# Performance work log

Hardware: AMD Instinct MI355X
Metric: run time of the kernel (lower is better)

The kernel has to match this reference:

```python
import jax, jax.numpy as jnp
import numpy as np

EPS = 1e-5  # torch BatchNorm2d default eps


def _bn(x, gamma, beta, mean, var):
    # inference-mode BatchNorm2d: x [B,C,H,W], params [C]
    inv = gamma / jnp.sqrt(var + EPS)
    return x * inv[None, :, None, None] + (beta - mean * inv)[None, :, None, None]


def _conv1x1(x, W, b=None):
    # 1x1 conv == per-pixel matmul. x [B,C,H,W], W [O,C]
    y = jnp.einsum('bchw,oc->bohw', x, W)
    if b is not None:
        y = y + b[None, :, None, None]
    return y


def _resize_bilinear_ac(x, H, W):
    # bilinear upsample with align_corners=True, separable gather + lerp
    h, w = x.shape[2], x.shape[3]
    ys = jnp.linspace(0.0, h - 1.0, H)
    xs = jnp.linspace(0.0, w - 1.0, W)
    y0 = jnp.floor(ys).astype(jnp.int32); y1 = jnp.minimum(y0 + 1, h - 1)
    x0 = jnp.floor(xs).astype(jnp.int32); x1 = jnp.minimum(x0 + 1, w - 1)
    wy = (ys - y0).astype(x.dtype)
    wx = (xs - x0).astype(x.dtype)
    rows = x[:, :, y0, :] * (1 - wy)[None, None, :, None] + x[:, :, y1, :] * wy[None, None, :, None]
    out = rows[:, :, :, x0] * (1 - wx) + rows[:, :, :, x1] * wx
    return out


def setup_inputs() -> dict:
    key = jax.random.key(0)
    ks = jax.random.split(key, 11)
    B, C, H, W = 8, 512, 96, 96
    Kd, Vd, Od = 256, 256, 512
    s = lambda k, shape: jax.random.normal(k, shape, jnp.float32)
    return dict(
        x=s(ks[0], (B, C, H, W)),
        Wk=s(ks[1], (Kd, C)) * 0.05,                      # shared query/key 1x1 conv
        k_gamma=jnp.ones((Kd,), jnp.float32), k_beta=jnp.zeros((Kd,), jnp.float32),
        k_mean=s(ks[2], (Kd,)) * 0.1, k_var=jnp.abs(s(ks[3], (Kd,))) + 0.5,
        Wv=s(ks[4], (Vd, C)) * 0.05, bv=s(ks[5], (Vd,)) * 0.05,   # value 1x1 conv
        Ww=s(ks[6], (Od, Vd)) * 0.05, bw=s(ks[7], (Od,)) * 0.05,  # 'weights' 1x1 conv (random instead of zero-init so output is nontrivial)
        Wr=s(ks[8], (Od, Od)) * 0.05,                             # refine 1x1 conv (in_dim==out_dim)
        r_gamma=jnp.ones((Od,), jnp.float32), r_beta=jnp.zeros((Od,), jnp.float32),
        r_mean=s(ks[9], (Od,)) * 0.1, r_var=jnp.abs(s(ks[10], (Od,))) + 0.5,
    )


def reference(x, Wk, k_gamma, k_beta, k_mean, k_var, Wv, bv, Ww, bw, Wr, r_gamma, r_beta, r_mean, r_var):
    B, C, H, W = x.shape
    scale = 2
    key_dim = Wk.shape[0]
    # MaxPool2d(scale, scale)
    xp = jax.lax.reduce_window(x, -jnp.inf, jax.lax.max,
                               (1, 1, scale, scale), (1, 1, scale, scale), 'VALID')
    h, w = xp.shape[2], xp.shape[3]
    N = h * w
    # query and key share the same conv+BN+ReLU (func_query = func_key)
    qk = jax.nn.relu(_bn(_conv1x1(xp, Wk), k_gamma, k_beta, k_mean, k_var)).reshape(B, key_dim, N)
    value = _conv1x1(xp, Wv, bv).reshape(B, -1, N)  # [B,Vd,N]
    # sim_map[b,n,m] = <query_n, key_m>, scaled then softmax over m
    sim = jnp.einsum('bkn,bkm->bnm', qk, qk) * (key_dim ** -0.5)
    attn = jax.nn.softmax(sim, axis=-1)
    ctx = jnp.einsum('bnm,bvm->bvn', attn, value).reshape(B, -1, h, w)  # [B,Vd,h,w]
    ctx = _conv1x1(ctx, Ww, bw)                      # -> [B,out_dim,h,w]
    ctx = _resize_bilinear_ac(ctx, H, W)             # align_corners=True bilinear
    out = jax.nn.relu(_bn(_conv1x1(ctx, Wr), r_gamma, r_beta, r_mean, r_var))
    return out
```

## Files before the change

kernel.cpp:

```cpp
#include <hip/hip_runtime.h>
#include <math.h>

typedef __attribute__((ext_vector_type(8))) short bf16x8;
typedef __attribute__((ext_vector_type(4))) float f32x4;

namespace {

constexpr int B_ = 8, C_ = 512, H_ = 96, W_ = 96;
constexpr int HP = 48, WP = 48, N_ = HP * WP;
constexpr int KD = 256, VD = 256, OD = 512;
constexpr int NSPLIT = 4;
constexpr float EPSV = 1e-5f;
constexpr float LOG2E = 1.44269504088896f;

constexpr size_t BOFF_XPT = 0;
constexpr size_t BOFF_QKT = BOFF_XPT + (size_t)B_ * N_ * C_ * 2;
constexpr size_t BOFF_VAL = BOFF_QKT + (size_t)B_ * N_ * KD * 2;
constexpr size_t BOFF_CTX = BOFF_VAL + (size_t)B_ * VD * N_ * 2;
constexpr size_t BOFF_W2  = BOFF_CTX + (size_t)B_ * N_ * VD * 2;
constexpr size_t BOFF_WF  = BOFF_W2  + (size_t)512 * 512 * 2;
constexpr size_t BOFF_BF  = BOFF_WF  + (size_t)OD * VD * 2;
constexpr size_t BOFF_PRT = BOFF_BF  + (size_t)OD * 4;
constexpr size_t BOFF_PM  = BOFF_PRT + (size_t)NSPLIT * B_ * N_ * VD * 2;
constexpr size_t BOFF_PL  = BOFF_PM  + (size_t)NSPLIT * B_ * N_ * 4;

}

__device__ __forceinline__ ushort f2bf(float f) {
    union { float f; unsigned u; } x; x.f = f;
    unsigned r = x.u + 0x7FFFu + ((x.u >> 16) & 1u);
    return (ushort)(r >> 16);
}

__device__ __forceinline__ float bf2f(ushort u) {
    union { unsigned u; float f; } x; x.u = ((unsigned)u) << 16;
    return x.f;
}

__device__ __forceinline__ void gload_lds16(const void* g, void* l) {
    __builtin_amdgcn_global_load_lds(
        (const __attribute__((address_space(1))) unsigned int*)g,
        (__attribute__((address_space(3))) unsigned int*)l, 16, 0, 0);
}

__global__ __launch_bounds__(192) void pool_t_kernel(const float* __restrict__ x,
                                                     ushort* __restrict__ xpT) {
    __shared__ float ps[64][49];
    const int gid = blockIdx.x;
    const int ct = gid & 7;
    const int tmp = gid >> 3;
    const int oh = tmp % 48;
    const int b  = tmp / 48;
    const int t = threadIdx.x;
    const int ow = t % 48, ci = t / 48;

    const int c0 = ct * 64;
#pragma unroll
    for (int pass = 0; pass < 16; ++pass) {
        const int c = pass * 4 + ci;
        const float* px = x + (((size_t)b * C_ + c0 + c) * H_ + 2 * oh) * W_ + 2 * ow;
        float2 a = *reinterpret_cast<const float2*>(px);
        float2 d = *reinterpret_cast<const float2*>(px + W_);
        ps[c][ow] = fmaxf(fmaxf(a.x, a.y), fmaxf(d.x, d.y));
    }
    __syncthreads();
    const int cc2 = (t & 31) * 2;
    const int nr0 = t >> 5;
#pragma unroll
    for (int pass = 0; pass < 8; ++pass) {
        const int nr = pass * 6 + nr0;
        ushort2 p2;
        p2.x = f2bf(ps[cc2][nr]);
        p2.y = f2bf(ps[cc2 + 1][nr]);
        *reinterpret_cast<ushort2*>(&xpT[((size_t)b * N_ + oh * 48 + nr) * C_ + c0 + cc2]) = p2;
    }
}

__global__ __launch_bounds__(256) void prep_kernel(const float* __restrict__ Wk,
                                                   const float* __restrict__ Wv,
                                                   const float* __restrict__ Wr,
                                                   const float* __restrict__ Ww,
                                                   const float* __restrict__ bw,
                                                   ushort* __restrict__ W2,
                                                   ushort* __restrict__ Wfb,
                                                   float* __restrict__ bfb) {
    const int blk = blockIdx.x;
    if (blk < 512) {
        const int m = blk;
        const float* src = (m < 256) ? (Wk + (size_t)m * 512) : (Wv + (size_t)(m - 256) * 512);
        const int k = threadIdx.x * 2;
        float2 v = *reinterpret_cast<const float2*>(src + k);
        ushort2 p; p.x = f2bf(v.x); p.y = f2bf(v.y);
        *reinterpret_cast<ushort2*>(&W2[(size_t)m * 512 + k]) = p;
    } else if (blk < 1024) {
        const int o = blk - 512;
        const int v = threadIdx.x;
        float s = 0.f;
        for (int c = 0; c < OD; ++c)
            s = fmaf(Wr[(size_t)o * OD + c], Ww[(size_t)c * VD + v], s);
        Wfb[(size_t)o * VD + v] = f2bf(s);
    } else {
        const int o = (blk - 1024) * 256 + threadIdx.x;
        float s = 0.f;
        for (int c = 0; c < OD; ++c) s = fmaf(Wr[(size_t)o * OD + c], bw[c], s);
        bfb[o] = s;
    }
}

__global__ __launch_bounds__(256) void qkv_mfma(
    const ushort* __restrict__ W2, const ushort* __restrict__ xpT,
    const float* __restrict__ kg, const float* __restrict__ kb,
    const float* __restrict__ km, const float* __restrict__ kv,
    const float* __restrict__ bv,
    ushort* __restrict__ qkT, ushort* __restrict__ val) {
    __shared__ ushort Al[2][4096];
    __shared__ ushort Bl[2][4096];

    const int id = blockIdx.x;
    const int b = id & 7;
    const int t = id >> 3;
    const int my = t & 7;
    const int nx = t >> 3;
    const int w = threadIdx.x >> 6, l = threadIdx.x & 63;
    const int lr = l & 15, lg = l >> 4;
    const int rbq = (lg * 8) ^ (((lr >> 1) & 3) << 3);

    const ushort* srcA = W2 + (size_t)(my * 64) * 512;
    const ushort* srcB = xpT + ((size_t)b * N_ + nx * 64) * 512;

    auto stage64 = [&](const ushort* src, int koff, char* lbase) {
#pragma unroll
        for (int j = 0; j < 2; ++j) {
            const int prow = j * 64 + w * 16 + (l >> 2);
            const int row = prow & 63;
            const int kc = prow >> 6;
            const int cb = ((l & 3) * 16) ^ (((row >> 1) & 3) << 4);
            const char* s = (const char*)(src + (size_t)row * 512 + koff) + kc * 64 + cb;
            gload_lds16(s, lbase + j * 4096 + w * 1024);
        }
    };

    stage64(srcA, 0, (char*)&Al[0][0]);
    stage64(srcB, 0, (char*)&Bl[0][0]);
    stage64(srcA, 64, (char*)&Al[1][0]);
    stage64(srcB, 64, (char*)&Bl[1][0]);

    f32x4 acc[4];
#pragma unroll
    for (int nt = 0; nt < 4; ++nt) acc[nt] = (f32x4){0.f, 0.f, 0.f, 0.f};

    for (int ks = 0; ks < 8; ++ks) {
        if (ks < 7) { asm volatile("s_waitcnt vmcnt(4)" ::: "memory"); }
        else        { asm volatile("s_waitcnt vmcnt(0)" ::: "memory"); }
        __builtin_amdgcn_s_barrier();
        __builtin_amdgcn_sched_barrier(0);
        const ushort* Ab = &Al[ks & 1][0];
        const ushort* Bb = &Bl[ks & 1][0];
        __builtin_amdgcn_s_setprio(1);
#pragma unroll
        for (int kc = 0; kc < 2; ++kc) {
            bf16x8 af = *reinterpret_cast<const bf16x8*>(Ab + kc * 2048 + (w * 16 + lr) * 32 + rbq);
#pragma unroll
            for (int nt = 0; nt < 4; ++nt) {
                bf16x8 bfr = *reinterpret_cast<const bf16x8*>(Bb + kc * 2048 + (nt * 16 + lr) * 32 + rbq);
                acc[nt] = __builtin_amdgcn_mfma_f32_16x16x32_bf16(af, bfr, acc[nt], 0, 0, 0);
            }
        }
        __builtin_amdgcn_s_setprio(0);
        __builtin_amdgcn_sched_barrier(0);
        __builtin_amdgcn_s_barrier();
        if (ks < 6) {
            stage64(srcA, (ks + 2) * 64, (char*)&Al[ks & 1][0]);
            stage64(srcB, (ks + 2) * 64, (char*)&Bl[ks & 1][0]);
        }
    }

    const int m0 = my * 64 + w * 16;
    if (m0 < 256) {
        float inv[4], add[4];
#pragma unroll
        for (int j = 0; j < 4; ++j) {
            int o = m0 + lg * 4 + j;
            inv[j] = kg[o] * rsqrtf(kv[o] + EPSV);
            add[j] = kb[o] - km[o] * inv[j];
        }
#pragma unroll
        for (int nt = 0; nt < 4; ++nt) {
            int n = nx * 64 + nt * 16 + lr;
            ushort4 q4;
            q4.x = f2bf(fmaxf(acc[nt][0] * inv[0] + add[0], 0.f));
            q4.y = f2bf(fmaxf(acc[nt][1] * inv[1] + add[1], 0.f));
            q4.z = f2bf(fmaxf(acc[nt][2] * inv[2] + add[2], 0.f));
            q4.w = f2bf(fmaxf(acc[nt][3] * inv[3] + add[3], 0.f));
            *reinterpret_cast<ushort4*>(&qkT[((size_t)b * N_ + n) * KD + m0 + lg * 4]) = q4;
        }
    } else {
#pragma unroll
        for (int j = 0; j < 4; ++j) {
            int vch = m0 - 256 + lg * 4 + j;
            float bb = bv[vch];
#pragma unroll
            for (int nt = 0; nt < 4; ++nt) {
                int n = nx * 64 + nt * 16 + lr;
                val[((size_t)b * VD + vch) * N_ + n] = f2bf(acc[nt][j] + bb);
            }
        }
    }
}

__global__ __launch_bounds__(256, 2) void attn_mfma(const ushort* __restrict__ qkT,
                                                    const ushort* __restrict__ val,
                                                    ushort* __restrict__ part,
                                                    float* __restrict__ pm,
                                                    float* __restrict__ pl) {
    __shared__ ushort Kl[2][8192];
    __shared__ ushort Vl[2][8192];
    __shared__ ushort Pl[4][512];

    const int id = blockIdx.x;
    const int b  = id & 7;
    const int rest = id >> 3;
    const int s  = rest & 3;
    const int qt = rest >> 2;
    const int q0 = qt * 64;
    const int t0 = s * 18;
    const int w  = threadIdx.x >> 6;
    const int l  = threadIdx.x & 63;
    const int lr = l & 15, lg = l >> 4;

    const ushort* Qb = qkT + (size_t)b * N_ * KD;
    const ushort* Vb = val + (size_t)b * VD * N_;

    const int rb = lr * 32 + ((lg * 8) ^ (((lr >> 1) & 3) << 3));

    bf16x8 qf[8];
    {
        const ushort* qrow = Qb + (size_t)(q0 + w * 16 + lr) * KD + lg * 8;
#pragma unroll
        for (int kc = 0; kc < 8; ++kc)
            qf[kc] = *reinterpret_cast<const bf16x8*>(qrow + kc * 32);
    }
    asm volatile("s_waitcnt vmcnt(0)" ::: "memory");

    auto stage_K = [&](int itx, int buf) {
#pragma unroll
        for (int j = 0; j < 4; ++j) {
            const int prow = j * 64 + w * 16 + (l >> 2);
            const int m = prow & 31;
            const int kc = prow >> 5;
            const int cb = ((l & 3) * 16) ^ (((m >> 1) & 3) << 4);
            const char* src = (const char*)Qb + (size_t)(itx * 32 + m) * (KD * 2) + kc * 64 + cb;
            gload_lds16(src, (char*)(&Kl[buf][0]) + j * 4096 + w * 1024);
        }
    };
    auto stage_V = [&](int itx, int buf) {
#pragma unroll
        for (int j = 0; j < 4; ++j) {
            const int r = j * 64 + w * 16 + (l >> 2);
            const int cb = ((l & 3) * 16) ^ (((r >> 1) & 3) << 4);
            const char* src = (const char*)Vb + (size_t)r * (N_ * 2) + itx * 64 + cb;
            gload_lds16(src, (char*)(&Vl[buf][0]) + j * 4096 + w * 1024);
        }
    };

    stage_K(t0, 0);
    stage_V(t0, 0);
    stage_K(t0 + 1, 1);

    f32x4 O[16];
#pragma unroll
    for (int vt = 0; vt < 16; ++vt) O[vt] = (f32x4){0.f, 0.f, 0.f, 0.f};
    f32x4 Ol = (f32x4){0.f, 0.f, 0.f, 0.f};
    float mrun[4] = {-1e30f, -1e30f, -1e30f, -1e30f};
    bf16x8 ones;
#pragma unroll
    for (int i = 0; i < 8; ++i) ones[i] = (short)0x3F80;

    const float SC = 0.0625f * LOG2E;
    ushort* Pw = &Pl[w][0];

    for (int it = 0; it < 18; ++it) {
        const int cur = it & 1;
        if (it < 17) { asm volatile("s_waitcnt vmcnt(8)" ::: "memory"); }
        else         { asm volatile("s_waitcnt vmcnt(4)" ::: "memory"); }
        __builtin_amdgcn_s_barrier();
        __builtin_amdgcn_sched_barrier(0);
        if (it < 17) stage_V(t0 + it + 1, cur ^ 1);

        const ushort* Kc = &Kl[cur][0];

        f32x4 S0 = (f32x4){0.f, 0.f, 0.f, 0.f};
        f32x4 S1 = (f32x4){0.f, 0.f, 0.f, 0.f};
        __builtin_amdgcn_s_setprio(1);
#pragma unroll
        for (int kc = 0; kc < 8; ++kc) {
            bf16x8 k0 = *reinterpret_cast<const bf16x8*>(Kc + kc * 1024 + rb);
            bf16x8 k1 = *reinterpret_cast<const bf16x8*>(Kc + kc * 1024 + 512 + rb);
            S0 = __builtin_amdgcn_mfma_f32_16x16x32_bf16(qf[kc], k0, S0, 0, 0, 0);
            S1 = __builtin_amdgcn_mfma_f32_16x16x32_bf16(qf[kc], k1, S1, 0, 0, 0);
        }
        __builtin_amdgcn_s_setprio(0);

        float s0[4], s1[4], mx[4];
        bool ok = true;
#pragma unroll
        for (int r = 0; r < 4; ++r) {
            s0[r] = S0[r] * SC;
            s1[r] = S1[r] * SC;
            float m2 = fmaxf(s0[r], s1[r]);
#pragma unroll
            for (int off = 1; off < 16; off <<= 1) m2 = fmaxf(m2, __shfl_xor(m2, off, 16));
            mx[r] = m2;
            ok = ok && (m2 <= mrun[r] + 11.5f);
        }
        if (!__all(ok)) {
            float corr[4];
#pragma unroll
            for (int r = 0; r < 4; ++r) {
                float mn = fmaxf(mrun[r], mx[r]);
                corr[r] = exp2f(mrun[r] - mn);
                mrun[r] = mn;
            }
#pragma unroll
            for (int vt = 0; vt < 16; ++vt) {
                f32x4 o = O[vt];
                o[0] *= corr[0]; o[1] *= corr[1]; o[2] *= corr[2]; o[3] *= corr[3];
                O[vt] = o;
            }
            Ol[0] *= corr[0]; Ol[1] *= corr[1]; Ol[2] *= corr[2]; Ol[3] *= corr[3];
        }
#pragma unroll
        for (int r = 0; r < 4; ++r) {
            const int row = lg * 4 + r;
            const int sw = ((row >> 1) & 3) << 3;
            Pw[row * 32 + (lr ^ sw)] = f2bf(exp2f(s0[r] - mrun[r]));
            Pw[row * 32 + ((16 + lr) ^ sw)] = f2bf(exp2f(s1[r] - mrun[r]));
        }

        if (it < 17) { asm volatile("s_waitcnt vmcnt(8)" ::: "memory"); }
        else         { asm volatile("s_waitcnt vmcnt(0)" ::: "memory"); }
        __builtin_amdgcn_s_barrier();
        __builtin_amdgcn_sched_barrier(0);
        if (it < 16) stage_K(t0 + it + 2, cur);

        bf16x8 pf = *reinterpret_cast<const bf16x8*>(Pw + rb);
        const ushort* Vc = &Vl[cur][0];
        __builtin_amdgcn_s_setprio(1);
        Ol = __builtin_amdgcn_mfma_f32_16x16x32_bf16(pf, ones, Ol, 0, 0, 0);
#pragma unroll
        for (int vt = 0; vt < 16; ++vt) {
            bf16x8 vf = *reinterpret_cast<const bf16x8*>(Vc + vt * 512 + rb);
            O[vt] = __builtin_amdgcn_mfma_f32_16x16x32_bf16(pf, vf, O[vt], 0, 0, 0);
        }
        __builtin_amdgcn_s_setprio(0);
    }

    float il[4];
#pragma unroll
    for (int r = 0; r < 4; ++r) il[r] = 1.0f / Ol[r];
    ushort* Pp = part + (((size_t)s * B_ + b) * N_ + q0 + w * 16) * VD;
#pragma unroll
    for (int vt = 0; vt < 16; ++vt) {
#pragma unroll
        for (int j = 0; j < 4; ++j)
            Pp[(size_t)(lg * 4 + j) * VD + vt * 16 + lr] = f2bf(O[vt][j] * il[j]);
    }
    if (lr == 0) {
#pragma unroll
        for (int r = 0; r < 4; ++r) {
            const size_t idx = ((size_t)s * B_ + b) * N_ + q0 + w * 16 + lg * 4 + r;
            pm[idx] = mrun[r];
            pl[idx] = Ol[r];
        }
    }
}

__global__ __launch_bounds__(256) void merge_kernel(const ushort* __restrict__ part,
                                                    const float* __restrict__ pm,
                                                    const float* __restrict__ pl,
                                                    ushort* __restrict__ ctxT) {
    const int row = blockIdx.x * 8 + (threadIdx.x >> 5);
    const int lane = threadIdx.x & 31;
    const size_t RN = (size_t)B_ * N_;

    float m[NSPLIT], lv[NSPLIT];
#pragma unroll
    for (int si = 0; si < NSPLIT; ++si) {
        m[si]  = pm[si * RN + row];
        lv[si] = pl[si * RN + row];
    }
    float M = fmaxf(fmaxf(m[0], m[1]), fmaxf(m[2], m[3]));
    float wgt[NSPLIT], wsum = 0.f;
#pragma unroll
    for (int si = 0; si < NSPLIT; ++si) {
        wgt[si] = exp2f(m[si] - M) * lv[si];
        wsum += wgt[si];
    }
    const float inv = 1.0f / wsum;

    float acc[8] = {};
#pragma unroll
    for (int si = 0; si < NSPLIT; ++si) {
        bf16x8 p = *reinterpret_cast<const bf16x8*>(&part[(si * RN + row) * VD + lane * 8]);
        const float ws = wgt[si];
#pragma unroll
        for (int j = 0; j < 8; ++j) acc[j] = fmaf(ws, bf2f((ushort)p[j]), acc[j]);
    }
    ushort4 o0, o1;
    o0.x = f2bf(acc[0] * inv); o0.y = f2bf(acc[1] * inv);
    o0.z = f2bf(acc[2] * inv); o0.w = f2bf(acc[3] * inv);
    o1.x = f2bf(acc[4] * inv); o1.y = f2bf(acc[5] * inv);
    o1.z = f2bf(acc[6] * inv); o1.w = f2bf(acc[7] * inv);
    ushort* dst = ctxT + (size_t)row * VD + lane * 8;
    *reinterpret_cast<ushort4*>(dst) = o0;
    *reinterpret_cast<ushort4*>(dst + 4) = o1;
}

__global__ __launch_bounds__(256) void out_mfma(const ushort* __restrict__ Wfb,
                                                const float* __restrict__ bfuse,
                                                const float* __restrict__ rg,
                                                const float* __restrict__ rbta,
                                                const float* __restrict__ rm,
                                                const float* __restrict__ rv,
                                                const ushort* __restrict__ ctxT,
                                                ushort* __restrict__ Z) {
    __shared__ ushort Al[2][4096];
    __shared__ ushort Bl[2][4096];

    const int id = blockIdx.x;
    const int b = id & 7;
    const int t = id >> 3;
    const int my = t & 7;
    const int nx = t >> 3;
    const int w = threadIdx.x >> 6, l = threadIdx.x & 63;
    const int lr = l & 15, lg = l >> 4;
    const int rbq = (lg * 8) ^ (((lr >> 1) & 3) << 3);

    const ushort* srcA = Wfb + (size_t)(my * 64) * VD;
    const ushort* srcB = ctxT + ((size_t)b * N_ + nx * 64) * VD;

    auto stage64 = [&](const ushort* src, int koff, char* lbase) {
#pragma unroll
        for (int j = 0; j < 2; ++j) {
            const int prow = j * 64 + w * 16 + (l >> 2);
            const int row = prow & 63;
            const int kc = prow >> 6;
            const int cb = ((l & 3) * 16) ^ (((row >> 1) & 3) << 4);
            const char* s = (const char*)(src + (size_t)row * VD + koff) + kc * 64 + cb;
            gload_lds16(s, lbase + j * 4096 + w * 1024);
        }
    };

    stage64(srcA, 0, (char*)&Al[0][0]);
    stage64(srcB, 0, (char*)&Bl[0][0]);
    stage64(srcA, 64, (char*)&Al[1][0]);
    stage64(srcB, 64, (char*)&Bl[1][0]);

    f32x4 acc[4];
#pragma unroll
    for (int nt = 0; nt < 4; ++nt) acc[nt] = (f32x4){0.f, 0.f, 0.f, 0.f};

    for (int ks = 0; ks < 4; ++ks) {
        if (ks < 3) { asm volatile("s_waitcnt vmcnt(4)" ::: "memory"); }
        else        { asm volatile("s_waitcnt vmcnt(0)" ::: "memory"); }
        __builtin_amdgcn_s_barrier();
        __builtin_amdgcn_sched_barrier(0);
        const ushort* Ab = &Al[ks & 1][0];
        const ushort* Bb = &Bl[ks & 1][0];
        __builtin_amdgcn_s_setprio(1);
#pragma unroll
        for (int kc = 0; kc < 2; ++kc) {
            bf16x8 af = *reinterpret_cast<const bf16x8*>(Ab + kc * 2048 + (w * 16 + lr) * 32 + rbq);
#pragma unroll
            for (int nt = 0; nt < 4; ++nt) {
                bf16x8 bfr = *reinterpret_cast<const bf16x8*>(Bb + kc * 2048 + (nt * 16 + lr) * 32 + rbq);
                acc[nt] = __builtin_amdgcn_mfma_f32_16x16x32_bf16(af, bfr, acc[nt], 0, 0, 0);
            }
        }
        __builtin_amdgcn_s_setprio(0);
        __builtin_amdgcn_sched_barrier(0);
        __builtin_amdgcn_s_barrier();
        if (ks < 2) {
            stage64(srcA, (ks + 2) * 64, (char*)&Al[ks & 1][0]);
            stage64(srcB, (ks + 2) * 64, (char*)&Bl[ks & 1][0]);
        }
    }

    const int m0 = my * 64 + w * 16;
#pragma unroll
    for (int j = 0; j < 4; ++j) {
        const int o = m0 + lg * 4 + j;
        const float inv = rg[o] * rsqrtf(rv[o] + EPSV);
        const float add = rbta[o] - rm[o] * inv;
        const float bb = bfuse[o];
#pragma unroll
        for (int nt = 0; nt < 4; ++nt) {
            const int n = nx * 64 + nt * 16 + lr;
            Z[((size_t)b * OD + o) * N_ + n] = f2bf((acc[nt][j] + bb) * inv + add);
        }
    }
}

__global__ void upsample_kernel(const ushort* __restrict__ Z,
                                float* __restrict__ out) {
    const int total = B_ * OD * H_ * (W_ / 4);
    const float s = 47.0f / 95.0f;
    for (int idx = blockIdx.x * blockDim.x + threadIdx.x; idx < total;
         idx += gridDim.x * blockDim.x) {
        const int xq = idx % 24;
        const int t = idx / 24;
        const int y = t % H_;
        const int bo = t / H_;
        const float fy = y * s;
        const int y0 = (int)fy;
        const int y1 = min(y0 + 1, HP - 1);
        const float wy = fy - y0;
        const ushort* Zp = Z + (size_t)bo * N_;
        const ushort* r0 = Zp + y0 * WP;
        const ushort* r1 = Zp + y1 * WP;
        float4 o4;
        float* po = &o4.x;
#pragma unroll
        for (int j = 0; j < 4; ++j) {
            const int x = xq * 4 + j;
            const float fx = x * s;
            const int x0 = (int)fx;
            const int x1 = min(x0 + 1, WP - 1);
            const float wx = fx - x0;
            float v00 = bf2f(r0[x0]), v01 = bf2f(r0[x1]);
            float v10 = bf2f(r1[x0]), v11 = bf2f(r1[x1]);
            float a = v00 + (v01 - v00) * wx;
            float c = v10 + (v11 - v10) * wx;
            po[j] = fmaxf(a + (c - a) * wy, 0.f);
        }
        *reinterpret_cast<float4*>(out + (size_t)idx * 4) = o4;
    }
}

extern "C" void kernel_launch(void* const* d_in, const int* in_sizes, int n_in,
                              void* d_out, int out_size, void* d_ws, size_t ws_size,
                              hipStream_t stream) {
    const float* x  = (const float*)d_in[0];
    const float* Wk = (const float*)d_in[1];
    const float* kg = (const float*)d_in[2];
    const float* kb = (const float*)d_in[3];
    const float* km = (const float*)d_in[4];
    const float* kvv= (const float*)d_in[5];
    const float* Wv = (const float*)d_in[6];
    const float* bv = (const float*)d_in[7];
    const float* Ww = (const float*)d_in[8];
    const float* bw = (const float*)d_in[9];
    const float* Wr = (const float*)d_in[10];
    const float* rg = (const float*)d_in[11];
    const float* rb = (const float*)d_in[12];
    const float* rm = (const float*)d_in[13];
    const float* rv = (const float*)d_in[14];

    char* wsb = (char*)d_ws;
    ushort* xpT  = (ushort*)(wsb + BOFF_XPT);
    ushort* qkT  = (ushort*)(wsb + BOFF_QKT);
    ushort* valp = (ushort*)(wsb + BOFF_VAL);
    ushort* ctxT = (ushort*)(wsb + BOFF_CTX);
    ushort* W2   = (ushort*)(wsb + BOFF_W2);
    ushort* Wfb  = (ushort*)(wsb + BOFF_WF);
    float*  bfb  = (float*)(wsb + BOFF_BF);
    ushort* part = (ushort*)(wsb + BOFF_PRT);
    float*  pm   = (float*)(wsb + BOFF_PM);
    float*  pl   = (float*)(wsb + BOFF_PL);
    ushort* Z    = (ushort*)(wsb + BOFF_XPT);
    float*  out  = (float*)d_out;

    pool_t_kernel<<<8 * 48 * 8, 192, 0, stream>>>(x, xpT);
    prep_kernel<<<1026, 256, 0, stream>>>(Wk, Wv, Wr, Ww, bw, W2, Wfb, bfb);
    qkv_mfma<<<2304, 256, 0, stream>>>(W2, xpT, kg, kb, km, kvv, bv, qkT, valp);
    attn_mfma<<<1152, 256, 0, stream>>>(qkT, valp, part, pm, pl);
    merge_kernel<<<(B_ * N_) / 8, 256, 0, stream>>>(part, pm, pl, ctxT);
    out_mfma<<<2304, 256, 0, stream>>>(Wfb, bfb, rg, rb, rm, rv, ctxT, Z);
    upsample_kernel<<<4096, 256, 0, stream>>>(Z, out);
}
```

Before: 293.8 us.

## Double query rows per attention wave and fold softmax scale into qk

Each attention wave now processes two 16-row query tiles (128 queries per block), so every K and V tile staged in LDS feeds twice as many MFMAs. The grid halves to 576 blocks. The softmax scale (1/16 * log2e) is folded into the qk projection by multiplying by its square root, which removes the per-score multiply. The 16-lane row-max shuffle now runs only on the rescale path, using the lane-local max for the threshold check. This raises register pressure (two O accumulator sets) and lowers block count and occupancy, and folding the scale into bf16 qk changes rounding slightly.

Result: slower. 335.2 us (+14.1%).

```diff
diff --git a/kernel.cpp b/kernel.cpp
--- a/kernel.cpp
+++ b/kernel.cpp
@@ -11,7 +11,7 @@
 constexpr int KD = 256, VD = 256, OD = 512;
 constexpr int NSPLIT = 4;
 constexpr float EPSV = 1e-5f;
-constexpr float LOG2E = 1.44269504088896f;
+constexpr float SCH = 0.30028060f;
 
 constexpr size_t BOFF_XPT = 0;
 constexpr size_t BOFF_QKT = BOFF_XPT + (size_t)B_ * N_ * C_ * 2;
@@ -188,10 +188,10 @@
         for (int nt = 0; nt < 4; ++nt) {
             int n = nx * 64 + nt * 16 + lr;
             ushort4 q4;
-            q4.x = f2bf(fmaxf(acc[nt][0] * inv[0] + add[0], 0.f));
-            q4.y = f2bf(fmaxf(acc[nt][1] * inv[1] + add[1], 0.f));
-            q4.z = f2bf(fmaxf(acc[nt][2] * inv[2] + add[2], 0.f));
-            q4.w = f2bf(fmaxf(acc[nt][3] * inv[3] + add[3], 0.f));
+            q4.x = f2bf(fmaxf(acc[nt][0] * inv[0] + add[0], 0.f) * SCH);
+            q4.y = f2bf(fmaxf(acc[nt][1] * inv[1] + add[1], 0.f) * SCH);
+            q4.z = f2bf(fmaxf(acc[nt][2] * inv[2] + add[2], 0.f) * SCH);
+            q4.w = f2bf(fmaxf(acc[nt][3] * inv[3] + add[3], 0.f) * SCH);
             *reinterpret_cast<ushort4*>(&qkT[((size_t)b * N_ + n) * KD + m0 + lg * 4]) = q4;
         }
     } else {
@@ -215,14 +215,14 @@
                                                     float* __restrict__ pl) {
     __shared__ ushort Kl[2][8192];
     __shared__ ushort Vl[2][8192];
-    __shared__ ushort Pl[4][512];
+    __shared__ ushort Pl[4][1024];
 
     const int id = blockIdx.x;
     const int b  = id & 7;
     const int rest = id >> 3;
     const int s  = rest & 3;
     const int qt = rest >> 2;
-    const int q0 = qt * 64;
+    const int q0 = qt * 128;
     const int t0 = s * 18;
     const int w  = threadIdx.x >> 6;
     const int l  = threadIdx.x & 63;
@@ -233,12 +233,13 @@
 
     const int rb = lr * 32 + ((lg * 8) ^ (((lr >> 1) & 3) << 3));
 
-    bf16x8 qf[8];
-    {
-        const ushort* qrow = Qb + (size_t)(q0 + w * 16 + lr) * KD + lg * 8;
+    bf16x8 qf[2][8];
+#pragma unroll
+    for (int u = 0; u < 2; ++u) {
+        const ushort* qrow = Qb + (size_t)(q0 + w * 32 + u * 16 + lr) * KD + lg * 8;
 #pragma unroll
         for (int kc = 0; kc < 8; ++kc)
-            qf[kc] = *reinterpret_cast<const bf16x8*>(qrow + kc * 32);
+            qf[u][kc] = *reinterpret_cast<const bf16x8*>(qrow + kc * 32);
     }
     asm volatile("s_waitcnt vmcnt(0)" ::: "memory");
 
@@ -267,16 +268,23 @@
     stage_V(t0, 0);
     stage_K(t0 + 1, 1);
 
-    f32x4 O[16];
-#pragma unroll
-    for (int vt = 0; vt < 16; ++vt) O[vt] = (f32x4){0.f, 0.f, 0.f, 0.f};
-    f32x4 Ol = (f32x4){0.f, 0.f, 0.f, 0.f};
-    float mrun[4] = {-1e30f, -1e30f, -1e30f, -1e30f};
+    f32x4 O[2][16];
+#pragma unroll
+    for (int u = 0; u < 2; ++u)
+#pragma unroll
+        for (int vt = 0; vt < 16; ++vt) O[u][vt] = (f32x4){0.f, 0.f, 0.f, 0.f};
+    f32x4 Ol[2];
+    Ol[0] = (f32x4){0.f, 0.f, 0.f, 0.f};
+    Ol[1] = (f32x4){0.f, 0.f, 0.f, 0.f};
+    float mrun[2][4];
+#pragma unroll
+    for (int u = 0; u < 2; ++u)
+#pragma unroll
+        for (int r = 0; r < 4; ++r) mrun[u][r] = -1e30f;
     bf16x8 ones;
 #pragma unroll
     for (int i = 0; i < 8; ++i) ones[i] = (short)0x3F80;
 
-    const float SC = 0.0625f * LOG2E;
     ushort* Pw = &Pl[w][0];
 
     for (int it = 0; it < 18; ++it) {
@@ -289,53 +297,65 @@
 
         const ushort* Kc = &Kl[cur][0];
 
-        f32x4 S0 = (f32x4){0.f, 0.f, 0.f, 0.f};
-        f32x4 S1 = (f32x4){0.f, 0.f, 0.f, 0.f};
+        f32x4 S0[2], S1[2];
+#pragma unroll
+        for (int u = 0; u < 2; ++u) {
+            S0[u] = (f32x4){0.f, 0.f, 0.f, 0.f};
+            S1[u] = (f32x4){0.f, 0.f, 0.f, 0.f};
+        }
         __builtin_amdgcn_s_setprio(1);
 #pragma unroll
         for (int kc = 0; kc < 8; ++kc) {
             bf16x8 k0 = *reinterpret_cast<const bf16x8*>(Kc + kc * 1024 + rb);
             bf16x8 k1 = *reinterpret_cast<const bf16x8*>(Kc + kc * 1024 + 512 + rb);
-            S0 = __builtin_amdgcn_mfma_f32_16x16x32_bf16(qf[kc], k0, S0, 0, 0, 0);
-            S1 = __builtin_amdgcn_mfma_f32_16x16x32_bf16(qf[kc], k1, S1, 0, 0, 0);
+            S0[0] = __builtin_amdgcn_mfma_f32_16x16x32_bf16(qf[0][kc], k0, S0[0], 0, 0, 0);
+            S0[1] = __builtin_amdgcn_mfma_f32_16x16x32_bf16(qf[1][kc], k0, S0[1], 0, 0, 0);
+            S1[0] = __builtin_amdgcn_mfma_f32_16x16x32_bf16(qf[0][kc], k1, S1[0], 0, 0, 0);
+            S1[1] = __builtin_amdgcn_mfma_f32_16x16x32_bf16(qf[1][kc], k1, S1[1], 0, 0, 0);
         }
         __builtin_amdgcn_s_setprio(0);
 
-        float s0[4], s1[4], mx[4];
         bool ok = true;
-#pragma unroll
-        for (int r = 0; r < 4; ++r) {
-            s0[r] = S0[r] * SC;
-            s1[r] = S1[r] * SC;
-            float m2 = fmaxf(s0[r], s1[r]);
-#pragma unroll
-            for (int off = 1; off < 16; off <<= 1) m2 = fmaxf(m2, __shfl_xor(m2, off, 16));
-            mx[r] = m2;
-            ok = ok && (m2 <= mrun[r] + 11.5f);
-        }
+        float lmax[2][4];
+#pragma unroll
+        for (int u = 0; u < 2; ++u)
+#pragma unroll
+            for (int r = 0; r < 4; ++r) {
+                lmax[u][r] = fmaxf(S0[u][r], S1[u][r]);
+                ok = ok && (lmax[u][r] <= mrun[u][r] + 11.5f);
+            }
         if (!__all(ok)) {
-            float corr[4];
+#pragma unroll
+            for (int u = 0; u < 2; ++u) {
+                float corr[4];
+#pragma unroll
+                for (int r = 0; r < 4; ++r) {
+                    float m2 = lmax[u][r];
+#pragma unroll
+                    for (int off = 1; off < 16; off <<= 1) m2 = fmaxf(m2, __shfl_xor(m2, off, 16));
+                    const float mn = fmaxf(mrun[u][r], m2);
+                    corr[r] = exp2f(mrun[u][r] - mn);
+                    mrun[u][r] = mn;
+                }
+#pragma unroll
+                for (int vt = 0; vt < 16; ++vt) {
+                    f32x4 o = O[u][vt];
+                    o[0] *= corr[0]; o[1] *= corr[1]; o[2] *= corr[2]; o[3] *= corr[3];
+                    O[u][vt] = o;
+                }
+                Ol[u][0] *= corr[0]; Ol[u][1] *= corr[1];
+                Ol[u][2] *= corr[2]; Ol[u][3] *= corr[3];
+            }
+        }
+#pragma unroll
+        for (int u = 0; u < 2; ++u)
 #pragma unroll
             for (int r = 0; r < 4; ++r) {
-                float mn = fmaxf(mrun[r], mx[r]);
-                corr[r] = exp2f(mrun[r] - mn);
-                mrun[r] = mn;
+                const int row = u * 16 + lg * 4 + r;
+                const int sw = ((row >> 1) & 3) << 3;
+                Pw[row * 32 + (lr ^ sw)] = f2bf(exp2f(S0[u][r] - mrun[u][r]));
+                Pw[row * 32 + ((16 + lr) ^ sw)] = f2bf(exp2f(S1[u][r] - mrun[u][r]));
             }
-#pragma unroll
-            for (int vt = 0; vt < 16; ++vt) {
-                f32x4 o = O[vt];
-                o[0] *= corr[0]; o[1] *= corr[1]; o[2] *= corr[2]; o[3] *= corr[3];
-                O[vt] = o;
-            }
-            Ol[0] *= corr[0]; Ol[1] *= corr[1]; Ol[2] *= corr[2]; Ol[3] *= corr[3];
-        }
-#pragma unroll
-        for (int r = 0; r < 4; ++r) {
-            const int row = lg * 4 + r;
-            const int sw = ((row >> 1) & 3) << 3;
-            Pw[row * 32 + (lr ^ sw)] = f2bf(exp2f(s0[r] - mrun[r]));
-            Pw[row * 32 + ((16 + lr) ^ sw)] = f2bf(exp2f(s1[r] - mrun[r]));
-        }
 
         if (it < 17) { asm volatile("s_waitcnt vmcnt(8)" ::: "memory"); }
         else         { asm volatile("s_waitcnt vmcnt(0)" ::: "memory"); }
@@ -343,34 +363,40 @@
         __builtin_amdgcn_sched_barrier(0);
         if (it < 16) stage_K(t0 + it + 2, cur);
 
-        bf16x8 pf = *reinterpret_cast<const bf16x8*>(Pw + rb);
+        bf16x8 pf0 = *reinterpret_cast<const bf16x8*>(Pw + rb);
+        bf16x8 pf1 = *reinterpret_cast<const bf16x8*>(Pw + 512 + rb);
         const ushort* Vc = &Vl[cur][0];
         __builtin_amdgcn_s_setprio(1);
-        Ol = __builtin_amdgcn_mfma_f32_16x16x32_bf16(pf, ones, Ol, 0, 0, 0);
+        Ol[0] = __builtin_amdgcn_mfma_f32_16x16x32_bf16(pf0, ones, Ol[0], 0, 0, 0);
+        Ol[1] = __builtin_amdgcn_mfma_f32_16x16x32_bf16(pf1, ones, Ol[1], 0, 0, 0);
 #pragma unroll
         for (int vt = 0; vt < 16; ++vt) {
             bf16x8 vf = *reinterpret_cast<const bf16x8*>(Vc + vt * 512 + rb);
-            O[vt] = __builtin_amdgcn_mfma_f32_16x16x32_bf16(pf, vf, O[vt], 0, 0, 0);
+            O[0][vt] = __builtin_amdgcn_mfma_f32_16x16x32_bf16(pf0, vf, O[0][vt], 0, 0, 0);
+            O[1][vt] = __builtin_amdgcn_mfma_f32_16x16x32_bf16(pf1, vf, O[1][vt], 0, 0, 0);
         }
         __builtin_amdgcn_s_setprio(0);
     }
 
-    float il[4];
-#pragma unroll
-    for (int r = 0; r < 4; ++r) il[r] = 1.0f / Ol[r];
-    ushort* Pp = part + (((size_t)s * B_ + b) * N_ + q0 + w * 16) * VD;
-#pragma unroll
-    for (int vt = 0; vt < 16; ++vt) {
-#pragma unroll
-        for (int j = 0; j < 4; ++j)
-            Pp[(size_t)(lg * 4 + j) * VD + vt * 16 + lr] = f2bf(O[vt][j] * il[j]);
-    }
-    if (lr == 0) {
-#pragma unroll
-        for (int r = 0; r < 4; ++r) {
-            const size_t idx = ((size_t)s * B_ + b) * N_ + q0 + w * 16 + lg * 4 + r;
-            pm[idx] = mrun[r];
-            pl[idx] = Ol[r];
+#pragma unroll
+    for (int u = 0; u < 2; ++u) {
+        float il[4];
+#pragma unroll
+        for (int r = 0; r < 4; ++r) il[r] = 1.0f / Ol[u][r];
+        ushort* Pp = part + (((size_t)s * B_ + b) * N_ + q0 + w * 32 + u * 16) * VD;
+#pragma unroll
+        for (int vt = 0; vt < 16; ++vt) {
+#pragma unroll
+            for (int j = 0; j < 4; ++j)
+                Pp[(size_t)(lg * 4 + j) * VD + vt * 16 + lr] = f2bf(O[u][vt][j] * il[j]);
+        }
+        if (lr == 0) {
+#pragma unroll
+            for (int r = 0; r < 4; ++r) {
+                const size_t idx = ((size_t)s * B_ + b) * N_ + q0 + w * 32 + u * 16 + lg * 4 + r;
+                pm[idx] = mrun[u][r];
+                pl[idx] = Ol[u][r];
+            }
         }
     }
 }
@@ -573,7 +599,7 @@
     pool_t_kernel<<<8 * 48 * 8, 192, 0, stream>>>(x, xpT);
     prep_kernel<<<1026, 256, 0, stream>>>(Wk, Wv, Wr, Ww, bw, W2, Wfb, bfb);
     qkv_mfma<<<2304, 256, 0, stream>>>(W2, xpT, kg, kb, km, kvv, bv, qkT, valp);
-    attn_mfma<<<1152, 256, 0, stream>>>(qkT, valp, part, pm, pl);
+    attn_mfma<<<576, 256, 0, stream>>>(qkT, valp, part, pm, pl);
     merge_kernel<<<(B_ * N_) / 8, 256, 0, stream>>>(part, pm, pl, ctxT);
     out_mfma<<<2304, 256, 0, stream>>>(Wfb, bfb, rg, rb, rm, rv, ctxT, Z);
     upsample_kernel<<<4096, 256, 0, stream>>>(Z, out);
```
